# Kernel tuning notes

Hardware: AMD Instinct MI355X
Metric: run time of the kernel (lower is better)

The kernel has to match this reference:

```python
import jax, jax.numpy as jnp
import numpy as np

N = 65536      # total nodes = B * MAXN
E = 524288     # edges (avg degree 8)
DX = 32; DG = 32
IN_DIM = DX + 3 * DG   # 128, after concat(x, g0, g1, g2)
H = 256; OUT = 8; MAXN = 8192


def setup_inputs() -> dict:
    key = jax.random.key(0)
    ks = jax.random.split(key, 40)
    inp = {}
    inp['x'] = jax.random.normal(ks[0], (N, DX), jnp.float32)
    inp['g0'] = jax.random.normal(ks[1], (N, DG), jnp.float32)
    inp['g1'] = jax.random.normal(ks[2], (N, DG), jnp.float32)
    inp['g2'] = jax.random.normal(ks[3], (N, DG), jnp.float32)
    inp['edge_src'] = jax.random.randint(ks[4], (E,), 0, N, jnp.int32)
    inp['edge_dst'] = jax.random.randint(ks[5], (E,), 0, N, jnp.int32)
    dims = [(IN_DIM, H), (H, H), (H, H), (H, H)]
    k = 6
    for i, (di, do) in enumerate(dims):
        s = 1.0 / np.sqrt(di)
        inp[f'Wl{i}'] = jax.random.uniform(ks[k], (di, do), jnp.float32, -s, s); k += 1
        inp[f'Wr{i}'] = jax.random.uniform(ks[k], (di, do), jnp.float32, -s, s); k += 1
        inp[f'b{i}'] = jnp.zeros((do,), jnp.float32)
    s = 1.0 / np.sqrt(MAXN)
    inp['mlp1_W1'] = jax.random.uniform(ks[k], (MAXN, H), jnp.float32, -s, s); k += 1
    inp['mlp1_b1'] = jnp.zeros((H,), jnp.float32)
    s = 1.0 / np.sqrt(H)
    inp['mlp1_W2'] = jax.random.uniform(ks[k], (H, 1), jnp.float32, -s, s); k += 1
    inp['mlp1_b2'] = jnp.zeros((1,), jnp.float32)
    inp['bn_gamma'] = jnp.ones((H,), jnp.float32)
    inp['bn_beta'] = jnp.zeros((H,), jnp.float32)
    inp['mlp2_W1'] = jax.random.uniform(ks[k], (H, H), jnp.float32, -s, s); k += 1
    inp['mlp2_b1'] = jnp.zeros((H,), jnp.float32)
    inp['mlp2_W2'] = jax.random.uniform(ks[k], (H, OUT), jnp.float32, -s, s); k += 1
    inp['mlp2_b2'] = jnp.zeros((OUT,), jnp.float32)
    return inp


def _forward(x, g0, g1, g2, edge_src, edge_dst,
             Wl0, Wr0, b0, Wl1, Wr1, b1, Wl2, Wr2, b2, Wl3, Wr3, b3,
             mlp1_W1, mlp1_b1, mlp1_W2, mlp1_b2, bn_gamma, bn_beta,
             mlp2_W1, mlp2_b1, mlp2_W2, mlp2_b2):
    h = jnp.concatenate([x, g0, g1, g2], axis=1)  # [N, IN_DIM]
    # mean-aggregation denominator (in-degree, clamped at 1 like PyG mean)
    cnt = jnp.maximum(
        jax.ops.segment_sum(jnp.ones((E,), h.dtype), edge_dst, num_segments=N), 1.0)
    for Wl, Wr, b in ((Wl0, Wr0, b0), (Wl1, Wr1, b1), (Wl2, Wr2, b2), (Wl3, Wr3, b3)):
        agg = jax.ops.segment_sum(h[edge_src], edge_dst, num_segments=N) / cnt[:, None]
        # SAGEConv: lin_l(mean of neighbors) + lin_r(self) + bias, then ReLU
        h = jax.nn.relu(agg @ Wl + h @ Wr + b)
        # F.dropout in eval / deterministic reference: identity
    h = h.reshape(-1, H, MAXN)                               # [B, H, MAXN]
    h = jax.nn.relu(jnp.einsum('bhm,mk->bhk', h, mlp1_W1) + mlp1_b1)
    h = (jnp.einsum('bhk,ko->bho', h, mlp1_W2) + mlp1_b2)[..., 0]  # [B, H]
    mean = h.mean(axis=0)
    var = h.var(axis=0)
    h = (h - mean) / jnp.sqrt(var + 1e-5) * bn_gamma + bn_beta
    h = jax.nn.relu(h)
    h = jax.nn.relu(h @ mlp2_W1 + mlp2_b1)
    return h @ mlp2_W2 + mlp2_b2                              # [B, OUT]


def reference(x, g0, g1, g2, edge_src, edge_dst,
              Wl0, Wr0, b0, Wl1, Wr1, b1, Wl2, Wr2, b2, Wl3, Wr3, b3,
              mlp1_W1, mlp1_b1, mlp1_W2, mlp1_b2, bn_gamma, bn_beta,
              mlp2_W1, mlp2_b1, mlp2_W2, mlp2_b2):
    return _forward(x, g0, g1, g2, edge_src, edge_dst,
                    Wl0, Wr0, b0, Wl1, Wr1, b1, Wl2, Wr2, b2, Wl3, Wr3, b3,
                    mlp1_W1, mlp1_b1, mlp1_W2, mlp1_b2, bn_gamma, bn_beta,
                    mlp2_W1, mlp2_b1, mlp2_W2, mlp2_b2)
```

## Files before the change

### kernel.cpp

```cpp
#include <hip/hip_runtime.h>
#include <hip/hip_bf16.h>


#define NN 65536
#define EE 524288
#define ROWS 65537
#define PCSR_CAP 720896

using frag16 = __attribute__((ext_vector_type(8))) short;
using f32x4  = __attribute__((ext_vector_type(4))) float;

__device__ __forceinline__ float b2f(unsigned short u) {
    union { unsigned u32; float f; } x; x.u32 = (unsigned)u << 16; return x.f;
}

__device__ __forceinline__ void gld_lds16(const void* g, void* l) {
    __builtin_amdgcn_global_load_lds(
        (const __attribute__((address_space(1))) void*)g,
        (__attribute__((address_space(3))) void*)l, 16, 0, 0);
}


__global__ void gs_zero_deg(int* deg) {
    int i = blockIdx.x * 256 + threadIdx.x;
    if (i < NN) deg[i] = 0;
}

__global__ void gs_zero_pad(__hip_bfloat16* P0, __hip_bfloat16* P1) {
    int i = blockIdx.x * 256 + threadIdx.x;
    P0[(size_t)NN * 512 + i] = __float2bfloat16(0.f);
    P1[(size_t)NN * 512 + i] = __float2bfloat16(0.f);
}

__global__ void gs_hist(const int* __restrict__ dst, int* __restrict__ deg) {
    int e = blockIdx.x * 256 + threadIdx.x;
    atomicAdd(&deg[dst[e]], 1);
}

__global__ void gs_fill(int* __restrict__ pcsr) {
    int i = blockIdx.x * 256 + threadIdx.x;
    if (i < PCSR_CAP) pcsr[i] = NN;
}

__global__ void gs_scan(const int* __restrict__ deg, int* __restrict__ prow,
                        int* __restrict__ cursor, float* __restrict__ inv_cnt) {
    __shared__ int part[1024];
    int t = threadIdx.x;
    int base = t * 64;
    int s = 0;
    for (int i = 0; i < 64; ++i) s += (deg[base + i] + 3) & ~3;
    part[t] = s;
    __syncthreads();
    for (int off = 1; off < 1024; off <<= 1) {
        int add = (t >= off) ? part[t - off] : 0;
        __syncthreads();
        part[t] += add;
        __syncthreads();
    }
    int run = (t == 0) ? 0 : part[t - 1];
    for (int i = 0; i < 64; ++i) {
        int n = base + i;
        int d = deg[n];
        prow[n] = run;
        cursor[n] = run;
        inv_cnt[n] = 1.0f / (float)(d > 0 ? d : 1);
        run += (d + 3) & ~3;
    }
    if (t == 1023) prow[NN] = run;
}

__global__ void gs_bucket(const int* __restrict__ src, const int* __restrict__ dst,
                          int* __restrict__ cursor, int* __restrict__ pcsr) {
    int e = blockIdx.x * 256 + threadIdx.x;
    int d = dst[e];
    int p = atomicAdd(&cursor[d], 1);
    pcsr[p] = src[e];
}

struct TcvtArgs {
    const float* src[8];
    __hip_bfloat16* dst[8];
    int ldk[8];
    int kofs[8];
    int kblk[8];
};

__global__ void gs_tcvt_all(TcvtArgs a) {
    int z = blockIdx.z;
    if ((int)blockIdx.x >= a.kblk[z]) return;
    const float* src = a.src[z];
    __hip_bfloat16* dst = a.dst[z];
    int ldk = a.ldk[z], kofs = a.kofs[z];
    __shared__ float tile[32][33];
    int kb = blockIdx.x * 32, nb = blockIdx.y * 32;
    int tx = threadIdx.x, ty = threadIdx.y;
#pragma unroll
    for (int i = 0; i < 32; i += 8)
        tile[ty + i][tx] = src[(size_t)(kb + ty + i) * 256 + nb + tx];
    __syncthreads();
#pragma unroll
    for (int i = 0; i < 32; i += 8) {
        int n = nb + ty + i, k = kb + tx;
        dst[(size_t)n * ldk + kofs + k] = __float2bfloat16(tile[tx][ty + i]);
    }
}

__global__ void gs_tcvt(const float* __restrict__ src, __hip_bfloat16* __restrict__ dst,
                        int ldk, int kofs) {
    __shared__ float tile[32][33];
    int kb = blockIdx.x * 32, nb = blockIdx.y * 32;
    int tx = threadIdx.x, ty = threadIdx.y;
#pragma unroll
    for (int i = 0; i < 32; i += 8)
        tile[ty + i][tx] = src[(size_t)(kb + ty + i) * 256 + nb + tx];
    __syncthreads();
#pragma unroll
    for (int i = 0; i < 32; i += 8) {
        int n = nb + ty + i, k = kb + tx;
        dst[(size_t)n * ldk + kofs + k] = __float2bfloat16(tile[tx][ty + i]);
    }
}

__global__ void gs_concat_bf(const float* __restrict__ x, const float* __restrict__ g0,
                             const float* __restrict__ g1, const float* __restrict__ g2,
                             __hip_bfloat16* __restrict__ h) {
    int idx = blockIdx.x * 256 + threadIdx.x;
    int n = idx >> 7, c = idx & 127;
    float v;
    if (c < 32)       v = x[n * 32 + c];
    else if (c < 64)  v = g0[n * 32 + (c - 32)];
    else if (c < 96)  v = g1[n * 32 + (c - 64)];
    else              v = g2[n * 32 + (c - 96)];
    h[(size_t)n * 512 + 256 + c] = __float2bfloat16(v);
}

template <int DIM>
__global__ void gs_agg_bf(const __hip_bfloat16* __restrict__ hsrc,
                          __hip_bfloat16* __restrict__ adst,
                          const int* __restrict__ prow, const int* __restrict__ pcsr,
                          const float* __restrict__ inv_cnt) {
    int wave = threadIdx.x >> 6;
    int lane = threadIdx.x & 63;
    int n = blockIdx.x * 4 + wave;
    int e = prow[n], pe = prow[n + 1];
    float iv = inv_cnt[n];
    if constexpr (DIM == 256) {
        const __hip_bfloat16* base = hsrc + lane * 4;
        float a0 = 0.f, a1 = 0.f, a2 = 0.f, a3 = 0.f;
        int4 s4;
        if (e < pe) s4 = *(const int4*)(pcsr + e);
        while (e < pe) {
            int4 cur = s4;
            e += 4;
            if (e < pe) s4 = *(const int4*)(pcsr + e);
            ushort4 v0 = *(const ushort4*)(base + (size_t)cur.x * 512);
            ushort4 v1 = *(const ushort4*)(base + (size_t)cur.y * 512);
            ushort4 v2 = *(const ushort4*)(base + (size_t)cur.z * 512);
            ushort4 v3 = *(const ushort4*)(base + (size_t)cur.w * 512);
            a0 += b2f(v0.x); a1 += b2f(v0.y); a2 += b2f(v0.z); a3 += b2f(v0.w);
            a0 += b2f(v1.x); a1 += b2f(v1.y); a2 += b2f(v1.z); a3 += b2f(v1.w);
            a0 += b2f(v2.x); a1 += b2f(v2.y); a2 += b2f(v2.z); a3 += b2f(v2.w);
            a0 += b2f(v3.x); a1 += b2f(v3.y); a2 += b2f(v3.z); a3 += b2f(v3.w);
        }
        __hip_bfloat16 o[4] = {__float2bfloat16(a0 * iv), __float2bfloat16(a1 * iv),
                               __float2bfloat16(a2 * iv), __float2bfloat16(a3 * iv)};
        *(ushort4*)(adst + (size_t)n * 512 + lane * 4) = *(const ushort4*)o;
    } else {
        const __hip_bfloat16* base = hsrc + lane * 2;
        float a0 = 0.f, a1 = 0.f;
        int4 s4;
        if (e < pe) s4 = *(const int4*)(pcsr + e);
        while (e < pe) {
            int4 cur = s4;
            e += 4;
            if (e < pe) s4 = *(const int4*)(pcsr + e);
            ushort2 v0 = *(const ushort2*)(base + (size_t)cur.x * 512);
            ushort2 v1 = *(const ushort2*)(base + (size_t)cur.y * 512);
            ushort2 v2 = *(const ushort2*)(base + (size_t)cur.z * 512);
            ushort2 v3 = *(const ushort2*)(base + (size_t)cur.w * 512);
            a0 += b2f(v0.x); a1 += b2f(v0.y);
            a0 += b2f(v1.x); a1 += b2f(v1.y);
            a0 += b2f(v2.x); a1 += b2f(v2.y);
            a0 += b2f(v3.x); a1 += b2f(v3.y);
        }
        __hip_bfloat16 o[2] = {__float2bfloat16(a0 * iv), __float2bfloat16(a1 * iv)};
        *(ushort2*)(adst + (size_t)n * 512 + lane * 2) = *(const ushort2*)o;
    }
}

__device__ __forceinline__ void mfma_block(const __hip_bfloat16* A, int lda,
                                           const __hip_bfloat16* Bt, int ldb,
                                           int kbeg, int kend, size_t row0, size_t nbase,
                                           __hip_bfloat16* As, __hip_bfloat16* Bs,
                                           f32x4 acc[4][4]) {
    const int t = threadIdx.x;
    const int lane = t & 63;
    const int w = t >> 6;
    const int wr = (w >> 1) * 64;
    const int wc = (w & 1) * 64;
    const int srow = w * 32 + (lane >> 3);
    const int scol = (lane & 7) * 8;
    for (int kc = kbeg; kc < kend; kc += 64) {
#pragma unroll
        for (int l = 0; l < 4; ++l) {
            gld_lds16(A + (row0 + srow + 8 * l) * (size_t)lda + kc + scol,
                      As + (w * 32 + 8 * l) * 64);
            gld_lds16(Bt + (nbase + srow + 8 * l) * (size_t)ldb + kc + scol,
                      Bs + (w * 32 + 8 * l) * 64);
        }
        __syncthreads();
#pragma unroll
        for (int kk = 0; kk < 64; kk += 32) {
            frag16 af[4], bf[4];
#pragma unroll
            for (int i = 0; i < 4; ++i)
                af[i] = *(const frag16*)(As + (wr + i * 16 + (lane & 15)) * 64 + kk + (lane >> 4) * 8);
#pragma unroll
            for (int j = 0; j < 4; ++j)
                bf[j] = *(const frag16*)(Bs + (wc + j * 16 + (lane & 15)) * 64 + kk + (lane >> 4) * 8);
#pragma unroll
            for (int i = 0; i < 4; ++i)
#pragma unroll
                for (int j = 0; j < 4; ++j)
                    acc[i][j] = __builtin_amdgcn_mfma_f32_16x16x32_bf16(af[i], bf[j], acc[i][j], 0, 0, 0);
        }
        __syncthreads();
    }
}

__global__ __launch_bounds__(256, 2)
void gs_gemm_bias_relu(const __hip_bfloat16* __restrict__ A, int lda, int K,
                       const __hip_bfloat16* __restrict__ Bt, int ldb,
                       const float* __restrict__ bias,
                       __hip_bfloat16* __restrict__ C, int ldc, int cofs) {
    __shared__ __hip_bfloat16 As[128 * 64];
    __shared__ __hip_bfloat16 Bs[128 * 64];
    f32x4 acc[4][4] = {};
    const size_t row0 = (size_t)blockIdx.x * 128;
    const size_t nbase = (size_t)blockIdx.y * 128;
    mfma_block(A, lda, Bt, ldb, 0, K, row0, nbase, As, Bs, acc);
    const int lane = threadIdx.x & 63;
    const int w = threadIdx.x >> 6;
    const int wr = (w >> 1) * 64, wc = (w & 1) * 64;
#pragma unroll
    for (int j = 0; j < 4; ++j) {
        int n = (int)nbase + wc + j * 16 + (lane & 15);
        float bv = bias[n];
#pragma unroll
        for (int i = 0; i < 4; ++i) {
#pragma unroll
            for (int r = 0; r < 4; ++r) {
                size_t row = row0 + wr + i * 16 + (lane >> 4) * 4 + r;
                C[row * (size_t)ldc + cofs + n] = __float2bfloat16(fmaxf(acc[i][j][r] + bv, 0.f));
            }
        }
    }
}

__global__ __launch_bounds__(256, 2)
void gs_gemm_splitk(const __hip_bfloat16* __restrict__ A, int lda,
                    const __hip_bfloat16* __restrict__ Bt, int ldb,
                    float* __restrict__ part) {
    __shared__ __hip_bfloat16 As[128 * 64];
    __shared__ __hip_bfloat16 Bs[128 * 64];
    f32x4 acc[4][4] = {};
    const size_t row0 = (size_t)blockIdx.x * 128;
    const size_t nbase = (size_t)blockIdx.y * 128;
    const int kbeg = blockIdx.z * 512;
    mfma_block(A, lda, Bt, ldb, kbeg, kbeg + 512, row0, nbase, As, Bs, acc);
    const int lane = threadIdx.x & 63;
    const int w = threadIdx.x >> 6;
    const int wr = (w >> 1) * 64, wc = (w & 1) * 64;
    float* p = part + (size_t)blockIdx.z * 2048 * 256;
#pragma unroll
    for (int j = 0; j < 4; ++j) {
        int n = (int)nbase + wc + j * 16 + (lane & 15);
#pragma unroll
        for (int i = 0; i < 4; ++i) {
#pragma unroll
            for (int r = 0; r < 4; ++r) {
                size_t row = row0 + wr + i * 16 + (lane >> 4) * 4 + r;
                p[row * 256 + n] = acc[i][j][r];
            }
        }
    }
}

__global__ void gs_mlp1_reduce(const float* __restrict__ part, const float* __restrict__ b1,
                               float* __restrict__ t1) {
    int idx = blockIdx.x * 256 + threadIdx.x;
    float s = 0.f;
#pragma unroll
    for (int ks = 0; ks < 16; ++ks) s += part[(size_t)ks * 524288 + idx];
    s += b1[idx & 255];
    t1[idx] = fmaxf(s, 0.f);
}

__global__ void gs_pool(const float* __restrict__ t1, const float* __restrict__ W2,
                        const float* __restrict__ b2, float* __restrict__ pooled) {
    int r = blockIdx.x;
    int l = threadIdx.x;
    float acc = 0.f;
#pragma unroll
    for (int q = 0; q < 4; ++q) {
        int c = l + q * 64;
        acc = fmaf(t1[(size_t)r * 256 + c], W2[c], acc);
    }
    for (int off = 32; off > 0; off >>= 1) acc += __shfl_down(acc, off);
    if (l == 0) pooled[r] = acc + b2[0];
}

__global__ void gs_bn_mlp2(const float* __restrict__ pooled, const float* __restrict__ gamma,
                           const float* __restrict__ beta, const float* __restrict__ W1,
                           const float* __restrict__ b1, const float* __restrict__ W2,
                           const float* __restrict__ b2, float* __restrict__ out) {
    __shared__ float hb[8][256];
    __shared__ float h2[8][256];
    int t = threadIdx.x;
    {
        float v[8];
        float m = 0.f;
#pragma unroll
        for (int b = 0; b < 8; ++b) { v[b] = pooled[b * 256 + t]; m += v[b]; }
        m *= 0.125f;
        float var = 0.f;
#pragma unroll
        for (int b = 0; b < 8; ++b) { float d = v[b] - m; var += d * d; }
        var *= 0.125f;
        float is = 1.0f / sqrtf(var + 1e-5f);
        float g = gamma[t], bt = beta[t];
#pragma unroll
        for (int b = 0; b < 8; ++b) hb[b][t] = fmaxf((v[b] - m) * is * g + bt, 0.f);
    }
    __syncthreads();
    {
        float acc[8] = {};
        for (int i = 0; i < 256; ++i) {
            float w = W1[i * 256 + t];
#pragma unroll
            for (int b = 0; b < 8; ++b) acc[b] = fmaf(hb[b][i], w, acc[b]);
        }
        float bb = b1[t];
#pragma unroll
        for (int b = 0; b < 8; ++b) h2[b][t] = fmaxf(acc[b] + bb, 0.f);
    }
    __syncthreads();
    if (t < 64) {
        int b = t >> 3, o = t & 7;
        float acc = 0.f;
        for (int j = 0; j < 256; ++j) acc = fmaf(h2[b][j], W2[j * 8 + o], acc);
        out[b * 8 + o] = acc + b2[o];
    }
}

extern "C" void kernel_launch(void* const* d_in, const int* in_sizes, int n_in,
                              void* d_out, int out_size, void* d_ws, size_t ws_size,
                              hipStream_t stream) {
    const float* x  = (const float*)d_in[0];
    const float* g0 = (const float*)d_in[1];
    const float* g1 = (const float*)d_in[2];
    const float* g2 = (const float*)d_in[3];
    const int* edge_src = (const int*)d_in[4];
    const int* edge_dst = (const int*)d_in[5];
    const float* Wl[4] = {(const float*)d_in[6], (const float*)d_in[9],
                          (const float*)d_in[12], (const float*)d_in[15]};
    const float* Wr[4] = {(const float*)d_in[7], (const float*)d_in[10],
                          (const float*)d_in[13], (const float*)d_in[16]};
    const float* bs[4] = {(const float*)d_in[8], (const float*)d_in[11],
                          (const float*)d_in[14], (const float*)d_in[17]};
    const float* mlp1_W1 = (const float*)d_in[18];
    const float* mlp1_b1 = (const float*)d_in[19];
    const float* mlp1_W2 = (const float*)d_in[20];
    const float* mlp1_b2 = (const float*)d_in[21];
    const float* bn_gamma = (const float*)d_in[22];
    const float* bn_beta  = (const float*)d_in[23];
    const float* mlp2_W1 = (const float*)d_in[24];
    const float* mlp2_b1 = (const float*)d_in[25];
    const float* mlp2_W2 = (const float*)d_in[26];
    const float* mlp2_b2 = (const float*)d_in[27];
    float* out = (float*)d_out;

    char* ws = (char*)d_ws;
    __hip_bfloat16* P0 = (__hip_bfloat16*)ws;
    __hip_bfloat16* P1 = P0 + (size_t)ROWS * 512;
    __hip_bfloat16* WC0 = P1 + (size_t)ROWS * 512;
    __hip_bfloat16* WC1 = WC0 + 65536;
    __hip_bfloat16* WC2 = WC1 + 131072;
    __hip_bfloat16* WC3 = WC2 + 131072;
    __hip_bfloat16* W1T = WC3 + 131072;
    float* inv_cnt = (float*)(W1T + 2097152);
    int* ideg = (int*)(inv_cnt + 65536);
    int* prow = ideg + 65536;
    int* cursor = prow + 65544;
    int* pcsr = cursor + 65536;
    __hip_bfloat16* H4 = P0;
    float* T1 = (float*)P1;
    float* pooled = T1 + 524288;
    float* PART = (float*)((char*)P1 + (size_t)(4 << 20));

    gs_zero_deg<<<256, 256, 0, stream>>>(ideg);
    gs_zero_pad<<<2, 256, 0, stream>>>(P0, P1);
    gs_hist<<<EE / 256, 256, 0, stream>>>(edge_dst, ideg);
    gs_scan<<<1, 1024, 0, stream>>>(ideg, prow, cursor, inv_cnt);
    gs_fill<<<(PCSR_CAP + 255) / 256, 256, 0, stream>>>(pcsr);
    gs_bucket<<<EE / 256, 256, 0, stream>>>(edge_src, edge_dst, cursor, pcsr);

    {
        TcvtArgs a;
        const float* srcs[8] = {Wl[0], Wr[0], Wl[1], Wr[1], Wl[2], Wr[2], Wl[3], Wr[3]};
        __hip_bfloat16* dsts[8] = {WC0, WC0, WC1, WC1, WC2, WC2, WC3, WC3};
        int ldks[8] = {256, 256, 512, 512, 512, 512, 512, 512};
        int kofss[8] = {0, 128, 0, 256, 0, 256, 0, 256};
        int kblks[8] = {4, 4, 8, 8, 8, 8, 8, 8};
        for (int i = 0; i < 8; ++i) {
            a.src[i] = srcs[i]; a.dst[i] = dsts[i];
            a.ldk[i] = ldks[i]; a.kofs[i] = kofss[i]; a.kblk[i] = kblks[i];
        }
        gs_tcvt_all<<<dim3(8, 8, 8), dim3(32, 8), 0, stream>>>(a);
    }
    gs_tcvt<<<dim3(256, 8), dim3(32, 8), 0, stream>>>(mlp1_W1, W1T, 8192, 0);

    gs_concat_bf<<<NN * 128 / 256, 256, 0, stream>>>(x, g0, g1, g2, P0);

    gs_agg_bf<128><<<NN / 4, 256, 0, stream>>>(P0 + 256, P0 + 128, prow, pcsr, inv_cnt);
    gs_gemm_bias_relu<<<dim3(NN / 128, 2), 256, 0, stream>>>(P0 + 128, 512, 256, WC0, 256,
                                                             bs[0], P1, 512, 256);
    gs_agg_bf<256><<<NN / 4, 256, 0, stream>>>(P1 + 256, P1, prow, pcsr, inv_cnt);
    gs_gemm_bias_relu<<<dim3(NN / 128, 2), 256, 0, stream>>>(P1, 512, 512, WC1, 512,
                                                             bs[1], P0, 512, 256);
    gs_agg_bf<256><<<NN / 4, 256, 0, stream>>>(P0 + 256, P0, prow, pcsr, inv_cnt);
    gs_gemm_bias_relu<<<dim3(NN / 128, 2), 256, 0, stream>>>(P0, 512, 512, WC2, 512,
                                                             bs[2], P1, 512, 256);
    gs_agg_bf<256><<<NN / 4, 256, 0, stream>>>(P1 + 256, P1, prow, pcsr, inv_cnt);
    gs_gemm_bias_relu<<<dim3(NN / 128, 2), 256, 0, stream>>>(P1, 512, 512, WC3, 512,
                                                             bs[3], H4, 256, 0);

    gs_gemm_splitk<<<dim3(16, 2, 16), 256, 0, stream>>>(H4, 8192, W1T, 8192, PART);
    gs_mlp1_reduce<<<2048, 256, 0, stream>>>(PART, mlp1_b1, T1);
    gs_pool<<<2048, 64, 0, stream>>>(T1, mlp1_W2, mlp1_b2, pooled);

    gs_bn_mlp2<<<1, 256, 0, stream>>>(pooled, bn_gamma, bn_beta, mlp2_W1, mlp2_b1,
                                      mlp2_W2, mlp2_b2, out);
}
```

Before: 557.8 us.

## Parallelize degree prefix scan across blocks and fold padding fills into it

The single-block 1024-thread serial-per-thread scan over node degrees becomes a three-kernel parallel scan: per-block reductions, a scan over 256 block sums, and a per-block apply. The apply kernel also writes the sentinel padding entries of the padded CSR directly, replacing the full-array fill kernel, and zeroes the pad rows of P0/P1, removing two small launches. The cost is one extra launch and slightly more complex indexing in exchange for a much more parallel preprocessing stage.

```diff
diff --git a/kernel.cpp b/kernel.cpp
--- a/kernel.cpp
+++ b/kernel.cpp
@@ -26,47 +26,66 @@
     if (i < NN) deg[i] = 0;
 }
 
-__global__ void gs_zero_pad(__hip_bfloat16* P0, __hip_bfloat16* P1) {
-    int i = blockIdx.x * 256 + threadIdx.x;
-    P0[(size_t)NN * 512 + i] = __float2bfloat16(0.f);
-    P1[(size_t)NN * 512 + i] = __float2bfloat16(0.f);
-}
-
 __global__ void gs_hist(const int* __restrict__ dst, int* __restrict__ deg) {
     int e = blockIdx.x * 256 + threadIdx.x;
     atomicAdd(&deg[dst[e]], 1);
 }
 
-__global__ void gs_fill(int* __restrict__ pcsr) {
-    int i = blockIdx.x * 256 + threadIdx.x;
-    if (i < PCSR_CAP) pcsr[i] = NN;
-}
-
-__global__ void gs_scan(const int* __restrict__ deg, int* __restrict__ prow,
-                        int* __restrict__ cursor, float* __restrict__ inv_cnt) {
-    __shared__ int part[1024];
+__global__ void gs_deg_reduce(const int* __restrict__ deg, int* __restrict__ bsum) {
     int t = threadIdx.x;
-    int base = t * 64;
-    int s = 0;
-    for (int i = 0; i < 64; ++i) s += (deg[base + i] + 3) & ~3;
-    part[t] = s;
-    __syncthreads();
-    for (int off = 1; off < 1024; off <<= 1) {
+    int p = (deg[blockIdx.x * 256 + t] + 3) & ~3;
+#pragma unroll
+    for (int off = 32; off > 0; off >>= 1) p += __shfl_down(p, off);
+    __shared__ int w4[4];
+    if ((t & 63) == 0) w4[t >> 6] = p;
+    __syncthreads();
+    if (t == 0) bsum[blockIdx.x] = w4[0] + w4[1] + w4[2] + w4[3];
+}
+
+__global__ void gs_scan_bsum(const int* __restrict__ bsum, int* __restrict__ bofs,
+                             int* __restrict__ prow) {
+    __shared__ int part[256];
+    int t = threadIdx.x;
+    int v = bsum[t];
+    part[t] = v;
+    __syncthreads();
+    for (int off = 1; off < 256; off <<= 1) {
         int add = (t >= off) ? part[t - off] : 0;
         __syncthreads();
         part[t] += add;
         __syncthreads();
     }
-    int run = (t == 0) ? 0 : part[t - 1];
-    for (int i = 0; i < 64; ++i) {
-        int n = base + i;
-        int d = deg[n];
-        prow[n] = run;
-        cursor[n] = run;
-        inv_cnt[n] = 1.0f / (float)(d > 0 ? d : 1);
-        run += (d + 3) & ~3;
-    }
-    if (t == 1023) prow[NN] = run;
+    bofs[t] = part[t] - v;
+    if (t == 255) prow[NN] = part[255];
+}
+
+__global__ void gs_scan_apply(const int* __restrict__ deg, const int* __restrict__ bofs,
+                              int* __restrict__ prow, int* __restrict__ cursor,
+                              float* __restrict__ inv_cnt, int* __restrict__ pcsr,
+                              __hip_bfloat16* __restrict__ P0,
+                              __hip_bfloat16* __restrict__ P1) {
+    __shared__ int part[256];
+    int t = threadIdx.x;
+    int i = blockIdx.x * 256 + t;
+    int d = deg[i];
+    int p = (d + 3) & ~3;
+    part[t] = p;
+    __syncthreads();
+    for (int off = 1; off < 256; off <<= 1) {
+        int add = (t >= off) ? part[t - off] : 0;
+        __syncthreads();
+        part[t] += add;
+        __syncthreads();
+    }
+    int beg = bofs[blockIdx.x] + part[t] - p;
+    prow[i] = beg;
+    cursor[i] = beg;
+    inv_cnt[i] = 1.0f / (float)(d > 0 ? d : 1);
+    for (int j = d; j < p; ++j) pcsr[beg + j] = NN;
+    if (blockIdx.x == 0) {
+        ((unsigned*)(P0 + (size_t)NN * 512))[t] = 0u;
+        ((unsigned*)(P1 + (size_t)NN * 512))[t] = 0u;
+    }
 }
 
 __global__ void gs_bucket(const int* __restrict__ src, const int* __restrict__ dst,
@@ -392,17 +411,19 @@
     int* ideg = (int*)(inv_cnt + 65536);
     int* prow = ideg + 65536;
     int* cursor = prow + 65544;
-    int* pcsr = cursor + 65536;
+    int* bsum = cursor + 65536;
+    int* bofs = bsum + 256;
+    int* pcsr = bofs + 256;
     __hip_bfloat16* H4 = P0;
     float* T1 = (float*)P1;
     float* pooled = T1 + 524288;
     float* PART = (float*)((char*)P1 + (size_t)(4 << 20));
 
     gs_zero_deg<<<256, 256, 0, stream>>>(ideg);
-    gs_zero_pad<<<2, 256, 0, stream>>>(P0, P1);
     gs_hist<<<EE / 256, 256, 0, stream>>>(edge_dst, ideg);
-    gs_scan<<<1, 1024, 0, stream>>>(ideg, prow, cursor, inv_cnt);
-    gs_fill<<<(PCSR_CAP + 255) / 256, 256, 0, stream>>>(pcsr);
+    gs_deg_reduce<<<256, 256, 0, stream>>>(ideg, bsum);
+    gs_scan_bsum<<<1, 256, 0, stream>>>(bsum, bofs, prow);
+    gs_scan_apply<<<256, 256, 0, stream>>>(ideg, bofs, prow, cursor, inv_cnt, pcsr, P0, P1);
     gs_bucket<<<EE / 256, 256, 0, stream>>>(edge_src, edge_dst, cursor, pcsr);
 
     {
```

Measured after the change: 516.0 us. 7.5% less time.
